# Performance work log

Measured on AMD Instinct MI355X. Metric: run time of the kernel, lower is better.

The kernel has to match this reference:

```python
import jax, jax.numpy as jnp
import numpy as np

B, S, H = 2, 2048, 2048
NH, NKV, HD = 16, 4, 128
ROPE_BASE = 10000.0


def hbit_linear(x, w):
    # BitNet: 8-bit per-token absmax activation quant, ternary (2-bit) weight quant
    s = 127.0 / jnp.clip(jnp.max(jnp.abs(x), axis=-1, keepdims=True), 1e-5, None)
    xq = jnp.clip(jnp.round(x * s), -128, 127) / s
    ws = 1.0 / jnp.clip(jnp.mean(jnp.abs(w)), 1e-5, None)
    wq = jnp.clip(jnp.round(w * ws), -1, 1) / ws
    return xq @ wq.T


def rotate_half(x):
    h = x.shape[-1] // 2
    return jnp.concatenate([-x[..., h:], x[..., :h]], axis=-1)


def rope_cos_sin(position_ids, head_dim, dtype):
    inv_freq = 1.0 / (ROPE_BASE ** (jnp.arange(0, head_dim, 2, dtype=jnp.float32) / head_dim))
    freqs = position_ids.astype(jnp.float32)[..., None] * inv_freq[None, None, :]  # (b,s,hd/2)
    emb = jnp.concatenate([freqs, freqs], axis=-1)  # (b,s,hd)
    return jnp.cos(emb).astype(dtype)[:, :, None, :], jnp.sin(emb).astype(dtype)[:, :, None, :]


def setup_inputs() -> dict:
    key = jax.random.key(0)
    ks = jax.random.split(key, 5)
    xavier = lambda k, shp: jax.random.uniform(k, shp, jnp.float32, -1.0, 1.0) * np.sqrt(6.0 / (shp[0] + shp[1]))
    causal = jnp.where(jnp.tril(jnp.ones((S, S), bool)), 0.0, -1e9).astype(jnp.float32)[None, None]
    return {
        "hidden_states": jax.random.normal(ks[0], (B, S, H), jnp.float32),
        "attention_mask": causal,
        "Wq": xavier(ks[1], (H, H)),
        "Wk": xavier(ks[2], (NKV * HD, H)),
        "Wv": xavier(ks[3], (NKV * HD, H)),
        "Wo": xavier(ks[4], (H, H)),
        "position_ids": jnp.arange(S, dtype=jnp.int64 if jax.config.jax_enable_x64 else jnp.int32)[None, :],
    }


def reference(hidden_states, attention_mask, Wq, Wk, Wv, Wo, position_ids):
    b, s, _ = hidden_states.shape
    q = hbit_linear(hidden_states, Wq).reshape(b, s, NH, HD)
    k = hbit_linear(hidden_states, Wk).reshape(b, s, NKV, HD)
    v = hbit_linear(hidden_states, Wv).reshape(b, s, NKV, HD)
    cos, sin = rope_cos_sin(position_ids, HD, q.dtype)  # (1,s,1,hd)
    q = q * cos + rotate_half(q) * sin
    k = k * cos + rotate_half(k) * sin
    n_rep = NH // NKV
    k = jnp.repeat(k, n_rep, axis=2)  # (b,s,NH,hd)
    v = jnp.repeat(v, n_rep, axis=2)
    scale = 1.0 / np.sqrt(HD)
    scores = jnp.einsum("bqhd,bkhd->bhqk", q, k) * scale + attention_mask
    probs = jax.nn.softmax(scores, axis=-1)  # dropout inactive (eval)
    out = jnp.einsum("bhqk,bkhd->bqhd", probs, v).reshape(b, s, NH * HD)
    return hbit_linear(out, Wo)
```

## Files before the change

### kernel.cpp

```cpp
#include <hip/hip_runtime.h>
#include <hip/hip_bf16.h>

#define B_ 2
#define S_ 2048
#define H_ 2048
#define NH_ 16
#define NKV_ 4
#define HD_ 128
#define M_ (B_*S_)
#define KVD_ (NKV_*HD_)

typedef signed char s8;
typedef __attribute__((ext_vector_type(8))) short short8;
typedef __attribute__((ext_vector_type(4))) float f32x4;
typedef __attribute__((ext_vector_type(4))) int int4v;

__device__ __forceinline__ float loadf(const void* p, long i, int isb){
  if (isb) return __bfloat162float(((const __hip_bfloat16*)p)[i]);
  return ((const float*)p)[i];
}

__device__ __forceinline__ unsigned short f2bf(float f){
  union { float f; unsigned u; } v; v.f = f;
  unsigned r = v.u + 0x7FFF + ((v.u >> 16) & 1);
  return (unsigned short)(r >> 16);
}

__device__ __forceinline__ float bf2f(unsigned short b){
  union { unsigned u; float f; } v; v.u = ((unsigned)b) << 16; return v.f;
}

__device__ __forceinline__ void gl2lds16(const void* g, void* l){
  __builtin_amdgcn_global_load_lds(
      (const __attribute__((address_space(1))) void*)g,
      (__attribute__((address_space(3))) void*)l, 16, 0, 0);
}

__global__ void k_detect(const unsigned int* x, int* flag){
  __shared__ int sh[256];
  int t = threadIdx.x, c = 0;
  for (int i = t; i < 2048; i += 256){
    unsigned e = (x[i] >> 7) & 0xFF;
    if (e >= 90 && e <= 150) c++;
  }
  sh[t] = c; __syncthreads();
  for (int k = 128; k > 0; k >>= 1){ if (t < k) sh[t] += sh[t+k]; __syncthreads(); }
  if (t == 0) flag[0] = (sh[0] > 1228) ? 1 : 0;
}

__global__ void k_prep(const void* Wq, const void* Wk, const void* Wv, const void* Wo,
                       const int* flag, float* wsum, float* ct, float* st){
  int bid = blockIdx.x, t = threadIdx.x;
  if (t < 64){
    float inv = exp2f(-(float)t * 0.20762050593045952f);
    float a = (float)bid * inv;
    float sn, cs; sincosf(a, &sn, &cs);
    ct[bid*64 + t] = cs; st[bid*64 + t] = sn;
  }
  __shared__ float sh[256];
  int isb = *flag;
  const void* w; long n; int wi; long b0; int nb;
  if (bid < 768)       { w = Wq; wi = 0; n = (long)H_*H_;   b0 = bid;      nb = 768; }
  else if (bid < 1024) { w = Wk; wi = 1; n = (long)KVD_*H_; b0 = bid-768;  nb = 256; }
  else if (bid < 1280) { w = Wv; wi = 2; n = (long)KVD_*H_; b0 = bid-1024; nb = 256; }
  else                 { w = Wo; wi = 3; n = (long)H_*H_;   b0 = bid-1280; nb = 768; }
  float s = 0.f;
  for (long i = b0*256 + t; i < n; i += (long)nb*256) s += fabsf(loadf(w, i, isb));
  sh[t] = s; __syncthreads();
  for (int k = 128; k > 0; k >>= 1){ if (t < k) sh[t] += sh[t+k]; __syncthreads(); }
  if (t == 0) atomicAdd(&wsum[wi], sh[0]);
}

__global__ void k_wquant_all(const void* Wq, const void* Wk, const void* Wv, const void* Wo,
                             const int* flag, const float* wsum,
                             s8* oq, s8* ok, s8* ov, s8* oo){
  int isb = *flag;
  int bid = blockIdx.x, t = threadIdx.x;
  const float cntq = (float)((long)H_*H_), cntkv = (float)((long)KVD_*H_);
  const void* w; s8* out; long n; int wi; long b0; int nb; float cnt;
  if (bid < 1024)      { w = Wq; out = oq; wi = 0; n = (long)H_*H_;   b0 = bid;       nb = 1024; cnt = cntq; }
  else if (bid < 1280) { w = Wk; out = ok; wi = 1; n = (long)KVD_*H_; b0 = bid-1024;  nb = 256;  cnt = cntkv; }
  else if (bid < 1536) { w = Wv; out = ov; wi = 2; n = (long)KVD_*H_; b0 = bid-1280;  nb = 256;  cnt = cntkv; }
  else                 { w = Wo; out = oo; wi = 3; n = (long)H_*H_;   b0 = bid-1536;  nb = 1024; cnt = cntq; }
  float mean = fmaxf(wsum[wi] / cnt, 1e-5f);
  float sc = 1.0f / mean;
  for (long i = b0*256 + t; i < n; i += (long)nb*256){
    float v = rintf(loadf(w, i, isb) * sc);
    v = fminf(fmaxf(v, -1.f), 1.f);
    out[i] = (s8)v;
  }
}

__global__ void k_aquant_in(const void* x, const int* flag, float* srow, s8* xq){
  __shared__ float sh[256];
  int isb = *flag; int r = blockIdx.x, t = threadIdx.x;
  long base = (long)r * H_;
  float v[8];
  if (isb){
    uint4 wv = ((const uint4*)((const unsigned short*)x + base))[t];
    unsigned u[4] = {wv.x, wv.y, wv.z, wv.w};
    #pragma unroll
    for (int i = 0; i < 4; i++){
      v[2*i]   = bf2f((unsigned short)(u[i] & 0xFFFF));
      v[2*i+1] = bf2f((unsigned short)(u[i] >> 16));
    }
  } else {
    const float4* p = (const float4*)((const float*)x + base);
    float4 a = p[t*2], b2 = p[t*2+1];
    v[0]=a.x; v[1]=a.y; v[2]=a.z; v[3]=a.w; v[4]=b2.x; v[5]=b2.y; v[6]=b2.z; v[7]=b2.w;
  }
  float mx = 0.f;
  #pragma unroll
  for (int i = 0; i < 8; i++) mx = fmaxf(mx, fabsf(v[i]));
  sh[t] = mx; __syncthreads();
  for (int k = 128; k > 0; k >>= 1){ if (t < k) sh[t] = fmaxf(sh[t], sh[t+k]); __syncthreads(); }
  float s = 127.0f / fmaxf(sh[0], 1e-5f);
  if (t == 0) srow[r] = s;
  unsigned long long pk = 0;
  #pragma unroll
  for (int i = 0; i < 8; i++){
    float q = fminf(fmaxf(rintf(v[i] * s), -128.f), 127.f);
    pk |= ((unsigned long long)(unsigned char)(s8)q) << (8*i);
  }
  *(unsigned long long*)(xq + base + t*8) = pk;
}

__global__ void k_aquant_bf16(const unsigned short* __restrict__ x, float* __restrict__ srow, s8* __restrict__ xq){
  __shared__ float sh[256];
  int r = blockIdx.x, t = threadIdx.x;
  long base = (long)r * H_;
  uint4 wv = ((const uint4*)(x + base))[t];
  unsigned u[4] = {wv.x, wv.y, wv.z, wv.w};
  float v[8];
  #pragma unroll
  for (int i = 0; i < 4; i++){
    v[2*i]   = bf2f((unsigned short)(u[i] & 0xFFFF));
    v[2*i+1] = bf2f((unsigned short)(u[i] >> 16));
  }
  float mx = 0.f;
  #pragma unroll
  for (int i = 0; i < 8; i++) mx = fmaxf(mx, fabsf(v[i]));
  sh[t] = mx; __syncthreads();
  for (int k = 128; k > 0; k >>= 1){ if (t < k) sh[t] = fmaxf(sh[t], sh[t+k]); __syncthreads(); }
  float s = 127.0f / fmaxf(sh[0], 1e-5f);
  if (t == 0) srow[r] = s;
  unsigned long long pk = 0;
  #pragma unroll
  for (int i = 0; i < 8; i++){
    float q = fminf(fmaxf(rintf(v[i] * s), -128.f), 127.f);
    pk |= ((unsigned long long)(unsigned char)(s8)q) << (8*i);
  }
  *(unsigned long long*)(xq + base + t*8) = pk;
}

__device__ __forceinline__ void gemm_core(
      const s8* __restrict__ A, const s8* __restrict__ Bw, s8* As, s8* Bs,
      const float* __restrict__ srow, float mean,
      void* __restrict__ Cout, int N, int mode, int isb,
      unsigned short* __restrict__ Vt,
      const float* __restrict__ ct, const float* __restrict__ st, long bcol){
  int tid = threadIdx.x;
  int wave = tid >> 6, lane = tid & 63;
  int quad = lane >> 4, c = lane & 15;
  int wm = wave >> 1, wn = wave & 1;
  long arow = (long)blockIdx.y * 128;
  const int K = H_;

  int4v acc[4][4];
  #pragma unroll
  for (int mt = 0; mt < 4; mt++)
    #pragma unroll
    for (int nt = 0; nt < 4; nt++) acc[mt][nt] = (int4v){0,0,0,0};

  int rl = lane >> 2;
  int kq = (lane & 3) ^ ((lane >> 3) & 3);
  int ch0 = wave*2, ch1 = wave*2 + 1;
  long gA0 = (arow + ch0*16 + rl)*(long)K + kq*16;
  long gA1 = (arow + ch1*16 + rl)*(long)K + kq*16;
  long gB0 = (bcol + ch0*16 + rl)*(long)K + kq*16;
  long gB1 = (bcol + ch1*16 + rl)*(long)K + kq*16;

  int sA = quad ^ ((c >> 1) & 3);
  int ntl[4];
  #pragma unroll
  for (int nt = 0; nt < 4; nt++) ntl[nt] = 2*wn + (nt & 1) + 4*(nt >> 1);
  int frA[4], frB[4];
  #pragma unroll
  for (int mt = 0; mt < 4; mt++) frA[mt] = (wm*64 + mt*16 + c)*64 + sA*16;
  #pragma unroll
  for (int nt = 0; nt < 4; nt++) frB[nt] = (ntl[nt]*16 + c)*64 + sA*16;

  for (int k0 = 0; k0 < K; k0 += 64){
    gl2lds16(A  + gA0 + k0, As + ch0*1024);
    gl2lds16(A  + gA1 + k0, As + ch1*1024);
    gl2lds16(Bw + gB0 + k0, Bs + ch0*1024);
    gl2lds16(Bw + gB1 + k0, Bs + ch1*1024);
    __syncthreads();
    int4v afr[4], bfr[4];
    #pragma unroll
    for (int mt = 0; mt < 4; mt++) afr[mt] = *(const int4v*)&As[frA[mt]];
    #pragma unroll
    for (int nt = 0; nt < 4; nt++) bfr[nt] = *(const int4v*)&Bs[frB[nt]];
    #pragma unroll
    for (int mt = 0; mt < 4; mt++)
      #pragma unroll
      for (int nt = 0; nt < 4; nt++)
        acc[mt][nt] = __builtin_amdgcn_mfma_i32_16x16x64_i8(afr[mt], bfr[nt], acc[mt][nt], 0, 0, 0);
    __syncthreads();
  }

  if (mode == 0 || mode == 3){
    unsigned short* Ob = (unsigned short*)Cout;
    #pragma unroll
    for (int mt = 0; mt < 4; mt++){
      #pragma unroll
      for (int r = 0; r < 4; r++){
        long grow = arow + wm*64 + mt*16 + quad*4 + r;
        float sc = mean / srow[grow];
        if (mode == 0) sc *= 0.08838834764831845f;
        int pos = (int)(grow & (S_-1));
        #pragma unroll
        for (int p = 0; p < 2; p++){
          int col_lo = (int)bcol + (2*wn + p)*16 + c;
          int d = col_lo & 63;
          float cv = ct[pos*64 + d], sv = st[pos*64 + d];
          float vlo = acc[mt][p][r]   * sc;
          float vhi = acc[mt][p+2][r] * sc;
          Ob[grow*(long)N + col_lo]      = f2bf(vlo*cv - vhi*sv);
          Ob[grow*(long)N + col_lo + 64] = f2bf(vhi*cv + vlo*sv);
        }
      }
    }
  } else if (mode == 1){
    #pragma unroll
    for (int mt = 0; mt < 4; mt++){
      #pragma unroll
      for (int r = 0; r < 4; r++){
        long grow = arow + wm*64 + mt*16 + quad*4 + r;
        float sc = mean / srow[grow];
        long bb = grow >> 11; int sI = (int)(grow & (S_-1));
        unsigned short* base = Vt + bb*(long)KVD_*S_ + sI;
        #pragma unroll
        for (int nt = 0; nt < 4; nt++)
          base[(long)(bcol + ntl[nt]*16 + c)*S_] = f2bf(acc[mt][nt][r] * sc);
      }
    }
  } else {
    #pragma unroll
    for (int mt = 0; mt < 4; mt++){
      #pragma unroll
      for (int r = 0; r < 4; r++){
        long grow = arow + wm*64 + mt*16 + quad*4 + r;
        float sc = mean / srow[grow];
        long cb = grow*(long)N + bcol + c;
        if (isb){
          __hip_bfloat16* o = (__hip_bfloat16*)Cout;
          #pragma unroll
          for (int nt = 0; nt < 4; nt++)
            o[cb + ntl[nt]*16] = __float2bfloat16(acc[mt][nt][r] * sc);
        } else {
          float* o = (float*)Cout;
          #pragma unroll
          for (int nt = 0; nt < 4; nt++)
            o[cb + ntl[nt]*16] = acc[mt][nt][r] * sc;
        }
      }
    }
  }
}

__global__ __launch_bounds__(256, 2) void k_gemm_qkv(
      const s8* __restrict__ xq,
      const s8* __restrict__ wqq, const s8* __restrict__ wkq, const s8* __restrict__ wvq,
      const float* __restrict__ srow, const float* __restrict__ wsum,
      unsigned short* __restrict__ Qb, unsigned short* __restrict__ Kb,
      unsigned short* __restrict__ Vt,
      const float* __restrict__ ct, const float* __restrict__ st){
  __shared__ __align__(16) s8 As[128*64];
  __shared__ __align__(16) s8 Bs[128*64];
  int bx = blockIdx.x;
  const float cntq = (float)((long)H_*H_), cntkv = (float)((long)KVD_*H_);
  const s8* Bw; void* Cout; unsigned short* vt = nullptr;
  int N, mode; float mean; long bcol;
  if (bx < 16){
    Bw = wqq; Cout = Qb; N = H_;   mode = 0; mean = fmaxf(wsum[0]/cntq, 1e-5f);  bcol = (long)bx*128;
  } else if (bx < 20){
    Bw = wkq; Cout = Kb; N = KVD_; mode = 3; mean = fmaxf(wsum[1]/cntkv, 1e-5f); bcol = (long)(bx-16)*128;
  } else {
    Bw = wvq; Cout = nullptr; vt = Vt; N = KVD_; mode = 1; mean = fmaxf(wsum[2]/cntkv, 1e-5f); bcol = (long)(bx-20)*128;
  }
  gemm_core(xq, Bw, As, Bs, srow, mean, Cout, N, mode, 0, vt, ct, st, bcol);
}

__global__ __launch_bounds__(256, 2) void k_gemm_o(
      const s8* __restrict__ aq, const s8* __restrict__ woq,
      const float* __restrict__ srow, const float* __restrict__ wsum,
      const int* __restrict__ flag, void* __restrict__ out,
      const float* __restrict__ ct, const float* __restrict__ st){
  __shared__ __align__(16) s8 As[128*64];
  __shared__ __align__(16) s8 Bs[128*64];
  float mean = fmaxf(wsum[3] / (float)((long)H_*H_), 1e-5f);
  gemm_core(aq, woq, As, Bs, srow, mean, out, H_, 2, *flag, nullptr, ct, st, (long)blockIdx.x*128);
}

#define PSTR 40
__global__ __launch_bounds__(256) void k_attn_mfma(const unsigned short* __restrict__ Qb,
    const unsigned short* __restrict__ Kb, const unsigned short* __restrict__ Vt,
    unsigned short* __restrict__ ob){
  int wid = threadIdx.x >> 6, lane = threadIdx.x & 63;
  int quad = lane >> 4, c = lane & 15;
  int kvh = blockIdx.y, b = blockIdx.z;
  int win = blockIdx.x;
  if (b == 1) win = (S_/32 - 1) - win;
  int h = kvh*4 + wid;
  int q0 = win*32;

  __shared__ __align__(16) unsigned short Ks[2][64*128];
  __shared__ __align__(16) unsigned short Vs[128*64];
  __shared__ __align__(16) unsigned short Ps[4][16*PSTR];

  short8 qf[2][4];
  #pragma unroll
  for (int t0 = 0; t0 < 2; t0++)
    #pragma unroll
    for (int f = 0; f < 4; f++)
      qf[t0][f] = *(const short8*)(Qb + ((long)(b*S_ + q0 + t0*16 + c)*NH_ + h)*HD_ + f*32 + quad*8);

  const unsigned short* Kg = Kb + (long)b*S_*KVD_ + kvh*HD_;
  const unsigned short* Vg = Vt + ((long)b*KVD_ + kvh*HD_)*S_;

  f32x4 o[2][8], ol[2];
  #pragma unroll
  for (int t0 = 0; t0 < 2; t0++){
    #pragma unroll
    for (int i = 0; i < 8; i++) o[t0][i] = (f32x4){0.f,0.f,0.f,0.f};
    ol[t0] = (f32x4){0.f,0.f,0.f,0.f};
  }
  short8 ones;
  #pragma unroll
  for (int i = 0; i < 8; i++) ones[i] = (short)0x3F80;

  int skey = lane >> 4;
  int kslot = lane & 15;
  int vrow = lane >> 3;
  int vslot = lane & 7;

  int nk = q0 + 32;
  #pragma unroll
  for (int i = 0; i < 4; i++){
    int kk = wid*16 + i*4;
    int key = kk + skey;
    int g = kslot ^ (key & 15);
    gl2lds16(Kg + (long)key*KVD_ + g*8, &Ks[0][kk*128]);
  }

  int buf = 0;
  for (int kc = 0; kc < nk; kc += 64, buf ^= 1){
    __syncthreads();
    #pragma unroll
    for (int i = 0; i < 4; i++){
      int rr = wid*32 + i*8;
      int hd = rr + vrow;
      int g = vslot ^ (hd & 7);
      gl2lds16(Vg + (long)hd*S_ + kc + g*8, &Vs[rr*64]);
    }

    f32x4 s[2][4];
    #pragma unroll
    for (int t0 = 0; t0 < 2; t0++)
      #pragma unroll
      for (int kt = 0; kt < 4; kt++) s[t0][kt] = (f32x4){0.f,0.f,0.f,0.f};
    #pragma unroll
    for (int kt = 0; kt < 4; kt++){
      short8 kf4[4];
      #pragma unroll
      for (int f = 0; f < 4; f++)
        kf4[f] = *(const short8*)&Ks[buf][(kt*16 + c)*128 + ((f*4 + quad) ^ c)*8];
      #pragma unroll
      for (int t0 = 0; t0 < 2; t0++)
        #pragma unroll
        for (int f = 0; f < 4; f++)
          s[t0][kt] = __builtin_amdgcn_mfma_f32_16x16x32_bf16(qf[t0][f], kf4[f], s[t0][kt], 0, 0, 0);
    }
    #pragma unroll
    for (int t0 = 0; t0 < 2; t0++){
      int qr0 = q0 + t0*16;
      if (kc + 63 > qr0){
        #pragma unroll
        for (int kt = 0; kt < 4; kt++){
          int key = kc + kt*16 + c;
          #pragma unroll
          for (int r = 0; r < 4; r++)
            if (key > qr0 + quad*4 + r) s[t0][kt][r] = -1e30f;
        }
      }
    }

    __syncthreads();

    if (kc + 64 < nk){
      #pragma unroll
      for (int i = 0; i < 4; i++){
        int kk = wid*16 + i*4;
        int key = kk + skey;
        int g = kslot ^ (key & 15);
        gl2lds16(Kg + (long)(kc + 64 + key)*KVD_ + g*8, &Ks[buf^1][kk*128]);
      }
    }

    #pragma unroll
    for (int pp = 0; pp < 2; pp++){
      short8 vf[8];
      #pragma unroll
      for (int nt = 0; nt < 8; nt++)
        vf[nt] = *(const short8*)&Vs[(nt*16 + c)*64 + ((pp*4 + quad) ^ (c & 7))*8];
      #pragma unroll
      for (int t0 = 0; t0 < 2; t0++){
        #pragma unroll
        for (int tk = 0; tk < 2; tk++)
          #pragma unroll
          for (int r = 0; r < 4; r++)
            Ps[wid][(quad*4 + r)*PSTR + tk*16 + c] = f2bf(__expf(s[t0][pp*2 + tk][r]));
        short8 pf = *(const short8*)&Ps[wid][c*PSTR + quad*8];
        #pragma unroll
        for (int nt = 0; nt < 8; nt++)
          o[t0][nt] = __builtin_amdgcn_mfma_f32_16x16x32_bf16(pf, vf[nt], o[t0][nt], 0, 0, 0);
        ol[t0] = __builtin_amdgcn_mfma_f32_16x16x32_bf16(pf, ones, ol[t0], 0, 0, 0);
      }
    }
  }

  #pragma unroll
  for (int t0 = 0; t0 < 2; t0++){
    float il[4];
    #pragma unroll
    for (int r = 0; r < 4; r++) il[r] = 1.0f / ol[t0][r];
    #pragma unroll
    for (int nt = 0; nt < 8; nt++)
      #pragma unroll
      for (int r = 0; r < 4; r++)
        ob[((long)(b*S_ + q0 + t0*16 + quad*4 + r))*H_ + h*HD_ + nt*16 + c] = f2bf(o[t0][nt][r]*il[r]);
  }
}

extern "C" void kernel_launch(void* const* d_in, const int* in_sizes, int n_in,
                              void* d_out, int out_size, void* d_ws, size_t ws_size,
                              hipStream_t stream){
  (void)in_sizes; (void)n_in; (void)out_size; (void)ws_size;
  const void* x  = d_in[0];
  const void* Wq = d_in[2];
  const void* Wk = d_in[3];
  const void* Wv = d_in[4];
  const void* Wo = d_in[5];
  char* ws = (char*)d_ws;
  size_t o = 0;
  auto alloc = [&](size_t b){ size_t r = o; o += (b + 255) & ~(size_t)255; return r; };
  size_t META = alloc(256);
  float* wsum = (float*)(ws + META);
  int*   flag = (int*)  (ws + META + 32);
  float* s_x = (float*)(ws + alloc((size_t)M_*4));
  float* s_a = (float*)(ws + alloc((size_t)M_*4));
  float* ct  = (float*)(ws + alloc((size_t)S_*64*4));
  float* st  = (float*)(ws + alloc((size_t)S_*64*4));
  s8* xq  = (s8*)(ws + alloc((size_t)M_*H_));
  s8* wqq = (s8*)(ws + alloc((size_t)H_*H_));
  s8* wkq = (s8*)(ws + alloc((size_t)KVD_*H_));
  s8* wvq = (s8*)(ws + alloc((size_t)KVD_*H_));
  s8* woq = (s8*)(ws + alloc((size_t)H_*H_));
  unsigned short* Qb = (unsigned short*)(ws + alloc((size_t)M_*NH_*HD_*2));
  unsigned short* Kb = (unsigned short*)(ws + alloc((size_t)M_*KVD_*2));
  unsigned short* Vt = (unsigned short*)(ws + alloc((size_t)M_*KVD_*2));
  unsigned short* ab = (unsigned short*)(ws + alloc((size_t)M_*H_*2));
  s8* aq = xq;

  hipMemsetAsync(ws + META, 0, 64, stream);
  k_detect<<<1,256,0,stream>>>((const unsigned int*)x, flag);
  k_prep<<<2048,256,0,stream>>>(Wq, Wk, Wv, Wo, flag, wsum, ct, st);
  k_wquant_all<<<2560,256,0,stream>>>(Wq, Wk, Wv, Wo, flag, wsum, wqq, wkq, wvq, woq);
  k_aquant_in<<<M_,256,0,stream>>>(x, flag, s_x, xq);

  dim3 gqkv(16+4+4, M_/128);
  k_gemm_qkv<<<gqkv, 256, 0, stream>>>(xq, wqq, wkq, wvq, s_x, wsum, Qb, Kb, Vt, ct, st);

  dim3 ga(S_/32, NKV_, B_);
  k_attn_mfma<<<ga, 256, 0, stream>>>(Qb, Kb, Vt, ab);

  k_aquant_bf16<<<M_,256,0,stream>>>(ab, s_a, aq);

  dim3 go(H_/128, M_/128);
  k_gemm_o<<<go, 256, 0, stream>>>(aq, woq, s_a, wsum, flag, d_out, ct, st);
}
```

Measured before the change: 314.1 us.

## Transpose QK^T MFMA operands, use exp2 with packed bf16 stores and setprio

The QK^T MFMA now takes its operands in swapped order, so each lane holds four consecutive keys for one query. The causal mask indexing is updated to match. The softmax scale is folded into log2(e)*scale in the Q epilogue so the kernel can use exp2f, and v_cvt_pk_bf16_f32 packs pairs of values that go to LDS as 8-byte stores instead of scalar 2-byte stores. s_setprio is placed around the MFMA blocks to favour matrix issue across waves. The aim is to cut exp cost, conversion instructions and LDS store count. The hardware bf16 conversion rounding may differ slightly from the software f2bf.

```diff
diff --git a/kernel.cpp b/kernel.cpp
--- a/kernel.cpp
+++ b/kernel.cpp
@@ -217,7 +217,7 @@
       for (int r = 0; r < 4; r++){
         long grow = arow + wm*64 + mt*16 + quad*4 + r;
         float sc = mean / srow[grow];
-        if (mode == 0) sc *= 0.08838834764831845f;
+        if (mode == 0) sc *= 0.12751743f;
         int pos = (int)(grow & (S_-1));
         #pragma unroll
         for (int p = 0; p < 2; p++){
@@ -376,22 +376,25 @@
       #pragma unroll
       for (int f = 0; f < 4; f++)
         kf4[f] = *(const short8*)&Ks[buf][(kt*16 + c)*128 + ((f*4 + quad) ^ c)*8];
+      __builtin_amdgcn_s_setprio(1);
       #pragma unroll
       for (int t0 = 0; t0 < 2; t0++)
         #pragma unroll
         for (int f = 0; f < 4; f++)
-          s[t0][kt] = __builtin_amdgcn_mfma_f32_16x16x32_bf16(qf[t0][f], kf4[f], s[t0][kt], 0, 0, 0);
+          s[t0][kt] = __builtin_amdgcn_mfma_f32_16x16x32_bf16(kf4[f], qf[t0][f], s[t0][kt], 0, 0, 0);
+      __builtin_amdgcn_s_setprio(0);
     }
     #pragma unroll
     for (int t0 = 0; t0 < 2; t0++){
-      int qr0 = q0 + t0*16;
-      if (kc + 63 > qr0){
+      int qv = q0 + t0*16 + c;
+      if (kc + 63 > q0 + t0*16){
         #pragma unroll
         for (int kt = 0; kt < 4; kt++){
-          int key = kc + kt*16 + c;
           #pragma unroll
-          for (int r = 0; r < 4; r++)
-            if (key > qr0 + quad*4 + r) s[t0][kt][r] = -1e30f;
+          for (int r = 0; r < 4; r++){
+            int key = kc + kt*16 + quad*4 + r;
+            if (key > qv) s[t0][kt][r] = -1e30f;
+          }
         }
       }
     }
@@ -417,15 +420,23 @@
       #pragma unroll
       for (int t0 = 0; t0 < 2; t0++){
         #pragma unroll
-        for (int tk = 0; tk < 2; tk++)
-          #pragma unroll
-          for (int r = 0; r < 4; r++)
-            Ps[wid][(quad*4 + r)*PSTR + tk*16 + c] = f2bf(__expf(s[t0][pp*2 + tk][r]));
+        for (int tk = 0; tk < 2; tk++){
+          f32x4 sv = s[t0][pp*2 + tk];
+          float e0 = exp2f(sv[0]), e1 = exp2f(sv[1]);
+          float e2 = exp2f(sv[2]), e3 = exp2f(sv[3]);
+          unsigned w0, w1;
+          asm("v_cvt_pk_bf16_f32 %0, %1, %2" : "=v"(w0) : "v"(e0), "v"(e1));
+          asm("v_cvt_pk_bf16_f32 %0, %1, %2" : "=v"(w1) : "v"(e2), "v"(e3));
+          uint2 pkv; pkv.x = w0; pkv.y = w1;
+          *(uint2*)&Ps[wid][c*PSTR + tk*16 + quad*4] = pkv;
+        }
         short8 pf = *(const short8*)&Ps[wid][c*PSTR + quad*8];
+        __builtin_amdgcn_s_setprio(1);
         #pragma unroll
         for (int nt = 0; nt < 8; nt++)
           o[t0][nt] = __builtin_amdgcn_mfma_f32_16x16x32_bf16(pf, vf[nt], o[t0][nt], 0, 0, 0);
         ol[t0] = __builtin_amdgcn_mfma_f32_16x16x32_bf16(pf, ones, ol[t0], 0, 0, 0);
+        __builtin_amdgcn_s_setprio(0);
       }
     }
   }
```

New measurement: 377.9 us. +20.3%, slower.
